# Kernel optimization log

Measured on AMD Instinct MI355X. Metric: run time of the kernel, lower is better.

Reference implementation:

```python
import jax, jax.numpy as jnp
import numpy as np

B, H, S, D = 4, 16, 1024, 64
MAX_REL = 128
VOCAB = 2 * MAX_REL + 1  # relative-position vocabulary


def setup_inputs() -> dict:
    key = jax.random.key(0)
    k1, k2, k3, k4 = jax.random.split(key, 4)
    tensor = jax.random.normal(k1, (B, H, S, D), dtype=jnp.float32)
    rel_keys_emb = jax.random.normal(k2, (VOCAB, D), dtype=jnp.float32) * 0.02
    rel_values_emb = jax.random.normal(k3, (VOCAB, D), dtype=jnp.float32) * 0.02
    # nn.Parameter initialized xavier_uniform_ on shape (1, H, 1, 1)
    bias = jax.random.uniform(k4, (1, H, 1, 1), dtype=jnp.float32, minval=-1.0, maxval=1.0)
    return {
        "tensor": tensor,
        "rel_keys_emb": rel_keys_emb,
        "rel_values_emb": rel_values_emb,
        "bias": bias,
        "max_relative_position": MAX_REL,
    }


def reference(tensor, rel_keys_emb, rel_values_emb, bias, max_relative_position):
    # forward(tensor, is_key=True, transpose=False)
    seq_len = tensor.shape[2]
    r = jnp.arange(seq_len)
    dist = jnp.clip(r[None, :] - r[:, None], -max_relative_position, max_relative_position)
    idx = dist + max_relative_position          # [S, S] in [0, 2*max_rel]
    rel_emb = rel_keys_emb[idx]                 # [S, S, D] gathered table
    # original: [S, B*H, D] @ [S, D, S] -> [S, B*H, S] -> [B, H, S, S]
    scores = jnp.einsum('bhsd,std->bhst', tensor, rel_emb)
    return scores + bias
```

## Files before the change

kernel.cpp:

```cpp
#include <hip/hip_runtime.h>


constexpr int S_     = 1024;
constexpr int D_     = 64;
constexpr int BQ     = 64;
constexpr int CPITCH = 276;

typedef __attribute__((ext_vector_type(8))) short short8;
typedef __attribute__((ext_vector_type(4))) float f32x4;

__device__ __forceinline__ unsigned short f2bf(float x) {
  unsigned u = __float_as_uint(x);
  return (unsigned short)((u + 0x7fffu + ((u >> 16) & 1u)) >> 16);
}
__device__ __forceinline__ short8 pack8(f32x4 a, f32x4 b) {
  short8 r;
  r[0] = (short)f2bf(a.x); r[1] = (short)f2bf(a.y);
  r[2] = (short)f2bf(a.z); r[3] = (short)f2bf(a.w);
  r[4] = (short)f2bf(b.x); r[5] = (short)f2bf(b.y);
  r[6] = (short)f2bf(b.z); r[7] = (short)f2bf(b.w);
  return r;
}
__device__ __forceinline__ f32x4 ntload4(const float* p) {
  return __builtin_nontemporal_load(reinterpret_cast<const f32x4*>(p));
}
__device__ __forceinline__ f32x4 ld4(const float* p) {
  return *reinterpret_cast<const f32x4*>(p);
}

__global__ __launch_bounds__(256, 4)
void relpos_v6(const float* __restrict__ tensor,
               const float* __restrict__ relk,
               const float* __restrict__ bias,
               float* __restrict__ out) {
  __shared__ __align__(16) unsigned short c_lds[BQ * CPITCH];

  const int tid  = threadIdx.x;
  const int lane = tid & 63;
  const int w    = tid >> 6;
  const int bh   = blockIdx.x >> 4;
  const int s0   = (blockIdx.x & 15) * BQ;
  const int h    = bh & 15;
  const int l15  = lane & 15;
  const int l4   = lane >> 4;
  const int r0   = 16 * w + l4 * 4;

  const float* xrow = tensor + ((size_t)(bh * S_ + s0 + 16 * w + l15)) * D_ + l4 * 8;
  short8 a0 = pack8(ntload4(xrow), ntload4(xrow + 4));
  short8 a1 = pack8(ntload4(xrow + 32), ntload4(xrow + 36));
  const float bv = bias[h];

#pragma unroll 2
  for (int nt = 0; nt < 17; ++nt) {
    const int vcol = 16 * nt + l15;
    const int erow = vcol > 256 ? 256 : vcol;
    const float* ep = relk + (size_t)erow * D_ + l4 * 8;
    short8 b0 = pack8(ld4(ep), ld4(ep + 4));
    short8 b1 = pack8(ld4(ep + 32), ld4(ep + 36));
    f32x4 acc = {0.f, 0.f, 0.f, 0.f};
    acc = __builtin_amdgcn_mfma_f32_16x16x32_bf16(a0, b0, acc, 0, 0, 0);
    acc = __builtin_amdgcn_mfma_f32_16x16x32_bf16(a1, b1, acc, 0, 0, 0);
    if (vcol <= 256) {
#pragma unroll
      for (int i = 0; i < 4; ++i)
        c_lds[(r0 + i) * CPITCH + i + 4 + vcol] = f2bf(acc[i] + bv);
    }
    if (l15 == 0 && nt == 0) {
#pragma unroll
      for (int i = 0; i < 4; ++i) {
        const unsigned short cv = f2bf(acc[i] + bv);
        for (int j = 0; j <= i + 3; ++j) c_lds[(r0 + i) * CPITCH + j] = cv;
      }
    }
    if (l15 == 0 && nt == 16) {
#pragma unroll
      for (int i = 0; i < 4; ++i) {
        const unsigned short cv = f2bf(acc[i] + bv);
        for (int j = i + 261; j < 268; ++j) c_lds[(r0 + i) * CPITCH + j] = cv;
      }
    }
  }
  __syncthreads();

  float* obase = out + ((size_t)bh * S_ + s0) * (size_t)S_;
  const int mc = 132 - s0;
#pragma unroll 4
  for (int it = 0; it < 64; ++it) {
    const int idx = it * 256 + tid;
    const int rl  = idx >> 8;
    const int t0  = (idx & 255) << 2;
    int m0 = t0 + (rl & 3) + mc - rl;
    m0 = m0 < 0 ? 0 : (m0 > 264 ? 264 : m0);
    const uint2 q = *reinterpret_cast<const uint2*>(&c_lds[rl * CPITCH + m0]);
    f32x4 o;
    o.x = __uint_as_float(q.x << 16);
    o.y = __uint_as_float(q.x & 0xffff0000u);
    o.z = __uint_as_float(q.y << 16);
    o.w = __uint_as_float(q.y & 0xffff0000u);
    __builtin_nontemporal_store(o, reinterpret_cast<f32x4*>(&obase[(size_t)idx * 4]));
  }
}

extern "C" void kernel_launch(void* const* d_in, const int* in_sizes, int n_in,
                              void* d_out, int out_size, void* d_ws, size_t ws_size,
                              hipStream_t stream) {
  const float* tensor = (const float*)d_in[0];
  const float* relk   = (const float*)d_in[1];
  const float* bias   = (const float*)d_in[3];
  float* out          = (float*)d_out;

  const int B = 4, H = 16;
  dim3 grid(B * H * (S_ / BQ));
  dim3 block(256);
  relpos_v6<<<grid, block, 0, stream>>>(tensor, relk, bias, out);
}
```

Measured before the change: 79.97 us.

## Process two row chunks per block with 16-byte LDS reads and wider stores

```diff
diff --git a/kernel.cpp b/kernel.cpp
--- a/kernel.cpp
+++ b/kernel.cpp
@@ -1,10 +1,11 @@
 #include <hip/hip_runtime.h>
 
 
-constexpr int S_     = 1024;
-constexpr int D_     = 64;
-constexpr int BQ     = 64;
-constexpr int CPITCH = 276;
+constexpr int S_ = 1024;
+constexpr int D_ = 64;
+constexpr int CP = 280;
+constexpr int ROWS = 64;
+constexpr int CHUNKS = 2;
 
 typedef __attribute__((ext_vector_type(8))) short short8;
 typedef __attribute__((ext_vector_type(4))) float f32x4;
@@ -12,6 +13,9 @@
 __device__ __forceinline__ unsigned short f2bf(float x) {
   unsigned u = __float_as_uint(x);
   return (unsigned short)((u + 0x7fffu + ((u >> 16) & 1u)) >> 16);
+}
+__device__ __forceinline__ f32x4 ld4(const float* p) {
+  return *reinterpret_cast<const f32x4*>(p);
 }
 __device__ __forceinline__ short8 pack8(f32x4 a, f32x4 b) {
   short8 r;
@@ -21,83 +25,91 @@
   r[6] = (short)f2bf(b.z); r[7] = (short)f2bf(b.w);
   return r;
 }
-__device__ __forceinline__ f32x4 ntload4(const float* p) {
-  return __builtin_nontemporal_load(reinterpret_cast<const f32x4*>(p));
-}
-__device__ __forceinline__ f32x4 ld4(const float* p) {
-  return *reinterpret_cast<const f32x4*>(p);
-}
 
-__global__ __launch_bounds__(256, 4)
-void relpos_v6(const float* __restrict__ tensor,
+__global__ __launch_bounds__(256, 1)
+void relpos_v8(const float* __restrict__ tensor,
                const float* __restrict__ relk,
                const float* __restrict__ bias,
                float* __restrict__ out) {
-  __shared__ __align__(16) unsigned short c_lds[BQ * CPITCH];
+  __shared__ __align__(16) unsigned short c_lds[ROWS * CP];
 
   const int tid  = threadIdx.x;
   const int lane = tid & 63;
   const int w    = tid >> 6;
-  const int bh   = blockIdx.x >> 4;
-  const int s0   = (blockIdx.x & 15) * BQ;
-  const int h    = bh & 15;
   const int l15  = lane & 15;
   const int l4   = lane >> 4;
   const int r0   = 16 * w + l4 * 4;
+  const int pb   = 4 * (l4 & 1);
 
-  const float* xrow = tensor + ((size_t)(bh * S_ + s0 + 16 * w + l15)) * D_ + l4 * 8;
-  short8 a0 = pack8(ntload4(xrow), ntload4(xrow + 4));
-  short8 a1 = pack8(ntload4(xrow + 32), ntload4(xrow + 36));
-  const float bv = bias[h];
+  for (int ch = 0; ch < CHUNKS; ++ch) {
+    const int cid = blockIdx.x * CHUNKS + ch;
+    const int bh  = cid >> 4;
+    const int s0  = (cid & 15) * ROWS;
+    const float bv = bias[bh & 15];
+
+    const float* xrow = tensor + ((size_t)(bh * S_ + s0 + 16 * w + l15)) * D_ + l4 * 8;
+    short8 a0 = pack8(ld4(xrow),      ld4(xrow + 4));
+    short8 a1 = pack8(ld4(xrow + 32), ld4(xrow + 36));
+
+    if (ch) __syncthreads();
 
 #pragma unroll 2
-  for (int nt = 0; nt < 17; ++nt) {
-    const int vcol = 16 * nt + l15;
-    const int erow = vcol > 256 ? 256 : vcol;
-    const float* ep = relk + (size_t)erow * D_ + l4 * 8;
-    short8 b0 = pack8(ld4(ep), ld4(ep + 4));
-    short8 b1 = pack8(ld4(ep + 32), ld4(ep + 36));
-    f32x4 acc = {0.f, 0.f, 0.f, 0.f};
-    acc = __builtin_amdgcn_mfma_f32_16x16x32_bf16(a0, b0, acc, 0, 0, 0);
-    acc = __builtin_amdgcn_mfma_f32_16x16x32_bf16(a1, b1, acc, 0, 0, 0);
-    if (vcol <= 256) {
+    for (int nt = 0; nt < 17; ++nt) {
+      const int vcol = 16 * nt + l15;
+      const int erow = vcol > 256 ? 256 : vcol;
+      const float* ep = relk + (size_t)erow * D_ + l4 * 8;
+      short8 b0 = pack8(ld4(ep),      ld4(ep + 4));
+      short8 b1 = pack8(ld4(ep + 32), ld4(ep + 36));
+      f32x4 acc = {0.f, 0.f, 0.f, 0.f};
+      acc = __builtin_amdgcn_mfma_f32_16x16x32_bf16(a0, b0, acc, 0, 0, 0);
+      acc = __builtin_amdgcn_mfma_f32_16x16x32_bf16(a1, b1, acc, 0, 0, 0);
+      if (vcol <= 256) {
 #pragma unroll
-      for (int i = 0; i < 4; ++i)
-        c_lds[(r0 + i) * CPITCH + i + 4 + vcol] = f2bf(acc[i] + bv);
-    }
-    if (l15 == 0 && nt == 0) {
+        for (int i = 0; i < 4; ++i)
+          c_lds[(r0 + i) * CP + pb + i + 8 + vcol] = f2bf(acc[i] + bv);
+      }
+      if (l15 == 0 && nt == 0) {
 #pragma unroll
-      for (int i = 0; i < 4; ++i) {
-        const unsigned short cv = f2bf(acc[i] + bv);
-        for (int j = 0; j <= i + 3; ++j) c_lds[(r0 + i) * CPITCH + j] = cv;
+        for (int i = 0; i < 4; ++i) {
+          const unsigned short cv = f2bf(acc[i] + bv);
+          const int pad = pb + i;
+          for (int j = 0; j <= pad + 7; ++j) c_lds[(r0 + i) * CP + j] = cv;
+        }
+      }
+      if (l15 == 0 && nt == 16) {
+#pragma unroll
+        for (int i = 0; i < 4; ++i) {
+          const unsigned short cv = f2bf(acc[i] + bv);
+          const int pad = pb + i;
+          for (int j = pad + 265; j < CP; ++j) c_lds[(r0 + i) * CP + j] = cv;
+        }
       }
     }
-    if (l15 == 0 && nt == 16) {
-#pragma unroll
-      for (int i = 0; i < 4; ++i) {
-        const unsigned short cv = f2bf(acc[i] + bv);
-        for (int j = i + 261; j < 268; ++j) c_lds[(r0 + i) * CPITCH + j] = cv;
-      }
+    __syncthreads();
+
+    float* obase = out + ((size_t)(bh * S_ + s0)) * (size_t)S_;
+    const int mc = 136 - s0;
+#pragma unroll 8
+    for (int it = 0; it < 32; ++it) {
+      const int idx = it * 256 + tid;
+      const int rl  = idx >> 7;
+      const int t0  = (idx & 127) << 3;
+      int m0 = t0 + (rl & 7) + mc - rl;
+      m0 = m0 < 0 ? 0 : (m0 > 272 ? 272 : m0);
+      const uint4 q = *reinterpret_cast<const uint4*>(&c_lds[rl * CP + m0]);
+      f32x4 o0, o1;
+      o0.x = __uint_as_float(q.x << 16);
+      o0.y = __uint_as_float(q.x & 0xffff0000u);
+      o0.z = __uint_as_float(q.y << 16);
+      o0.w = __uint_as_float(q.y & 0xffff0000u);
+      o1.x = __uint_as_float(q.z << 16);
+      o1.y = __uint_as_float(q.z & 0xffff0000u);
+      o1.z = __uint_as_float(q.w << 16);
+      o1.w = __uint_as_float(q.w & 0xffff0000u);
+      float* p = obase + ((size_t)rl << 10) + t0;
+      *reinterpret_cast<f32x4*>(p)     = o0;
+      *reinterpret_cast<f32x4*>(p + 4) = o1;
     }
-  }
-  __syncthreads();
-
-  float* obase = out + ((size_t)bh * S_ + s0) * (size_t)S_;
-  const int mc = 132 - s0;
-#pragma unroll 4
-  for (int it = 0; it < 64; ++it) {
-    const int idx = it * 256 + tid;
-    const int rl  = idx >> 8;
-    const int t0  = (idx & 255) << 2;
-    int m0 = t0 + (rl & 3) + mc - rl;
-    m0 = m0 < 0 ? 0 : (m0 > 264 ? 264 : m0);
-    const uint2 q = *reinterpret_cast<const uint2*>(&c_lds[rl * CPITCH + m0]);
-    f32x4 o;
-    o.x = __uint_as_float(q.x << 16);
-    o.y = __uint_as_float(q.x & 0xffff0000u);
-    o.z = __uint_as_float(q.y << 16);
-    o.w = __uint_as_float(q.y & 0xffff0000u);
-    __builtin_nontemporal_store(o, reinterpret_cast<f32x4*>(&obase[(size_t)idx * 4]));
   }
 }
 
@@ -109,8 +121,7 @@
   const float* bias   = (const float*)d_in[3];
   float* out          = (float*)d_out;
 
-  const int B = 4, H = 16;
-  dim3 grid(B * H * (S_ / BQ));
+  dim3 grid(512);
   dim3 block(256);
-  relpos_v6<<<grid, block, 0, stream>>>(tensor, relk, bias, out);
+  relpos_v8<<<grid, block, 0, stream>>>(tensor, relk, bias, out);
 }
```

New measurement: 72.97 us. 8.7% less time.
